# Optimization experiments

Hardware: AMD Instinct MI355X
Metric: run time of the kernel (lower is better)

The kernel has to match this reference:

```python
import jax, jax.numpy as jnp
import numpy as np

# config constants
H = 1024          # hidden_size
I = 512           # moe_intermediate_size
IS = 1024         # moe_shared_expert_intermediate_size
E = 16            # n_routed_experts
G = 4             # n_group
TOPK_G = 2        # topk_group
TOPK = 4          # num_experts_per_tok
SCALE = 2.5       # routed_scaling_factor
B, S = 2, 1024


def _relu2(x):
    r = jax.nn.relu(x)
    return r * r


def setup_inputs() -> dict:
    key = jax.random.key(0)
    ks = jax.random.split(key, 8)
    sd = 0.02
    return {
        "hidden_states": jax.random.normal(ks[0], (B, S, H), jnp.float32),
        "Wg": jax.random.normal(ks[1], (E, H), jnp.float32) * sd,          # router gate weight
        "bias_corr": jax.random.normal(ks[2], (E,), jnp.float32) * 0.01,    # e_score_correction_bias
        "W1": jax.random.normal(ks[3], (E, I, H), jnp.float32) * sd,        # experts up_proj
        "W2": jax.random.normal(ks[4], (E, H, I), jnp.float32) * sd,        # experts down_proj
        "Ws1": jax.random.normal(ks[5], (IS, H), jnp.float32) * sd,         # shared up_proj
        "Ws2": jax.random.normal(ks[6], (H, IS), jnp.float32) * sd,         # shared down_proj
    }


def _route(scores, bias_corr):
    # scores: (T,E) = sigmoid(router logits)
    T = scores.shape[0]
    s_choice = scores + bias_corr                                           # (T,E)
    gs = s_choice.reshape(T, G, E // G)
    group_scores = jnp.sum(jax.lax.top_k(gs, 2)[0], axis=-1)                # (T,G) sum of top-2 per group
    gidx = jax.lax.top_k(group_scores, TOPK_G)[1]                           # (T,topk_group)
    gmask = jnp.sum(jax.nn.one_hot(gidx, G, dtype=scores.dtype), axis=1)    # (T,G)
    smask = jnp.repeat(gmask, E // G, axis=1)                               # (T,E)
    masked = jnp.where(smask > 0, s_choice, 0.0)
    topk_idx = jax.lax.top_k(masked, TOPK)[1]                               # (T,top_k)
    topk_w = jnp.take_along_axis(scores, topk_idx, axis=1)                  # weights from raw sigmoid scores
    topk_w = topk_w / (jnp.sum(topk_w, axis=-1, keepdims=True) + 1e-20)     # norm_topk_prob
    topk_w = topk_w * SCALE
    return topk_idx, topk_w


def reference(hidden_states, Wg, bias_corr, W1, W2, Ws1, Ws2):
    b, s, h = hidden_states.shape
    flat = hidden_states.reshape(-1, h)                                     # (T,H)
    T = flat.shape[0]
    logits = flat.astype(jnp.float32) @ Wg.T                                # (T,E)
    scores = jax.nn.sigmoid(logits)
    topk_idx, topk_w = _route(scores, bias_corr)
    topk_w = topk_w.astype(hidden_states.dtype)
    # combined per-(token, expert) weight; zero where not routed (equivalent
    # to the per-expert gather/MLP/weighted index_add in the original)
    cw = jnp.zeros((T, E), flat.dtype)
    cw = cw.at[jnp.arange(T)[:, None], topk_idx].add(topk_w)                # (T,E)
    # fc1_latent_proj / fc2_latent_proj are Identity (moe_latent_size=None)
    hid = _relu2(jnp.einsum('th,eih->eti', flat, W1))                       # (E,T,I)
    y = jnp.einsum('eti,ehi->eth', hid, W2)                                 # (E,T,H)
    out = jnp.einsum('eth,te->th', y, cw)                                   # (T,H)
    shared = _relu2(flat @ Ws1.T) @ Ws2.T                                   # shared expert on residuals
    return (out + shared).reshape(b, s, h)
```

## Files before the change

### kernel.cpp

```cpp
#include <hip/hip_runtime.h>
#include <hip/hip_bf16.h>

#define T_TOK 2048
#define HDIM 1024
#define IDIM 512
#define ISDIM 1024
#define NEXP 16
#define TOPK 4
#define NSLOT (T_TOK*TOPK)
#define SCALE_F 2.5f

typedef unsigned short u16;
typedef float f32x4 __attribute__((ext_vector_type(4)));
typedef __bf16 bf16x8 __attribute__((ext_vector_type(8)));
typedef u16 u16x8 __attribute__((ext_vector_type(8)));

__device__ __forceinline__ u16 f2bf(float f) {
  unsigned u = __builtin_bit_cast(unsigned, f);
  u += 0x7fffu + ((u >> 16) & 1u);
  return (u16)(u >> 16);
}

__device__ __forceinline__ float bf2f(u16 h) {
  unsigned u = ((unsigned)h) << 16;
  return __builtin_bit_cast(float, u);
}

__device__ __forceinline__ void gload_lds16(const u16* g, u16* l) {
  __builtin_amdgcn_global_load_lds(
      (const __attribute__((address_space(1))) void*)g,
      (__attribute__((address_space(3))) void*)l, 16, 0, 0);
}

__device__ __forceinline__ f32x4 mfma16(u16x8 a, u16x8 b, f32x4 c) {
  return __builtin_amdgcn_mfma_f32_16x16x32_bf16(
      __builtin_bit_cast(bf16x8, a), __builtin_bit_cast(bf16x8, b), c, 0, 0, 0);
}

__device__ __forceinline__ void wait_vm6()   { asm volatile("s_waitcnt vmcnt(6)" ::: "memory"); }
__device__ __forceinline__ void wait_vm0()   { asm volatile("s_waitcnt vmcnt(0)" ::: "memory"); }
__device__ __forceinline__ void wait_lgkm0() { asm volatile("s_waitcnt lgkmcnt(0)" ::: "memory"); }

#define JMAX0 136
#define G0T (8*JMAX0)
#define JMAX1 240
#define G1T (8*JMAX1)
#define MAXG0 96
#define MAXG1 192

__global__ void __launch_bounds__(256) router_kernel(
    const float* __restrict__ x, const float* __restrict__ Wg,
    const float* __restrict__ bias,
    int* __restrict__ topk_idx, float* __restrict__ topk_w,
    u16* __restrict__ Xbf,
    int* __restrict__ counts, int* __restrict__ gfill) {
  int t = blockIdx.x;
  int tid = threadIdx.x;
  int lane = tid & 63;
  int wave = tid >> 6;

  if (t == 0 && tid < NEXP) { counts[tid] = 0; gfill[tid] = 0; }

  __shared__ __align__(16) float sx[HDIM];
  __shared__ float ssc[NEXP];

  float4 xv = reinterpret_cast<const float4*>(x + (size_t)t * HDIM)[tid];
  reinterpret_cast<float4*>(sx)[tid] = xv;
  ushort4 o;
  o.x = f2bf(xv.x); o.y = f2bf(xv.y); o.z = f2bf(xv.z); o.w = f2bf(xv.w);
  reinterpret_cast<ushort4*>(Xbf + (size_t)t * HDIM)[tid] = o;
  __syncthreads();

  float acc[4] = {0.f, 0.f, 0.f, 0.f};
  const float4* sx4 = reinterpret_cast<const float4*>(sx);
#pragma unroll
  for (int c = 0; c < 4; c++) {
    float4 xq = sx4[lane + 64 * c];
#pragma unroll
    for (int e = 0; e < 4; e++) {
      float4 wq = reinterpret_cast<const float4*>(
          Wg + (size_t)(wave * 4 + e) * HDIM)[lane + 64 * c];
      acc[e] += xq.x * wq.x + xq.y * wq.y + xq.z * wq.z + xq.w * wq.w;
    }
  }
#pragma unroll
  for (int e = 0; e < 4; e++) {
    float v = acc[e];
#pragma unroll
    for (int off = 32; off > 0; off >>= 1) v += __shfl_xor(v, off);
    if (lane == 0) ssc[wave * 4 + e] = v;
  }
  __syncthreads();

  if (tid == 0) {
    float scores[NEXP], sc[NEXP];
#pragma unroll
    for (int e = 0; e < NEXP; e++) {
      float s = 1.f / (1.f + expf(-ssc[e]));
      scores[e] = s;
      sc[e] = s + bias[e];
    }
    float gsum[4];
#pragma unroll
    for (int g = 0; g < 4; g++) {
      float a = sc[4*g], b = sc[4*g+1], c = sc[4*g+2], d = sc[4*g+3];
      float hi1 = fmaxf(a, b), lo1 = fminf(a, b);
      float hi2 = fmaxf(c, d), lo2 = fminf(c, d);
      gsum[g] = fmaxf(hi1, hi2) + fmaxf(fminf(hi1, hi2), fmaxf(lo1, lo2));
    }
    int g0 = 0; float bv = gsum[0];
#pragma unroll
    for (int g = 1; g < 4; g++) if (gsum[g] > bv) { bv = gsum[g]; g0 = g; }
    int g1 = -1; float bv2 = -1e30f;
#pragma unroll
    for (int g = 0; g < 4; g++) if (g != g0 && gsum[g] > bv2) { bv2 = gsum[g]; g1 = g; }
    float m[NEXP];
#pragma unroll
    for (int e = 0; e < NEXP; e++) {
      int g = e >> 2;
      m[e] = (g == g0 || g == g1) ? sc[e] : 0.0f;
    }
    int idx[TOPK]; float w[TOPK];
#pragma unroll
    for (int k = 0; k < TOPK; k++) {
      int bj = 0; float bmv = m[0];
#pragma unroll
      for (int j = 1; j < NEXP; j++) if (m[j] > bmv) { bmv = m[j]; bj = j; }
      idx[k] = bj; w[k] = scores[bj];
#pragma unroll
      for (int j = 0; j < NEXP; j++) m[j] = (j == bj) ? -1e30f : m[j];
    }
    float s4 = w[0] + w[1] + w[2] + w[3] + 1e-20f;
    float inv = SCALE_F / s4;
#pragma unroll
    for (int k = 0; k < TOPK; k++) {
      topk_idx[t * TOPK + k] = idx[k];
      topk_w[t * TOPK + k] = w[k] * inv;
    }
  }
}

__global__ void __launch_bounds__(256) hist_kernel(
    const int* __restrict__ topk_idx, int* __restrict__ counts) {
  int j = blockIdx.x * 256 + threadIdx.x;
  int lane = threadIdx.x & 63;
  int e = topk_idx[j];
  unsigned long long m = ~0ull;
#pragma unroll
  for (int b = 0; b < 4; b++) {
    unsigned long long bb = __ballot((e >> b) & 1);
    m &= ((e >> b) & 1) ? bb : ~bb;
  }
  int leader = __ffsll(m) - 1;
  if (lane == leader) atomicAdd(&counts[e], __popcll(m));
}

__global__ void __launch_bounds__(256) scatter_build(
    const int* __restrict__ topk_idx, const float* __restrict__ topk_w,
    const int* __restrict__ counts, int* __restrict__ offsets,
    int* __restrict__ gfill,
    int* __restrict__ perm_token, float* __restrict__ perm_w,
    int* __restrict__ slot_of,
    int* __restrict__ tiles0, int* __restrict__ tiles1) {
  int b = blockIdx.x;
  int tid = threadIdx.x;
  int lane = tid & 63;

  if (b < 32) {
    int c = (lane < NEXP) ? counts[lane] : 0;
    int incl = c;
#pragma unroll
    for (int o = 1; o < 16; o <<= 1) {
      int v = __shfl_up(incl, o);
      if (lane >= o) incl += v;
    }
    int excl = incl - c;

    int j = b * 256 + tid;
    int e = topk_idx[j];
    unsigned long long m = ~0ull;
#pragma unroll
    for (int bb = 0; bb < 4; bb++) {
      unsigned long long bl = __ballot((e >> bb) & 1);
      m &= ((e >> bb) & 1) ? bl : ~bl;
    }
    int leader = __ffsll(m) - 1;
    int rank = __popcll(m & ((1ull << lane) - 1ull));
    int base = 0;
    if (lane == leader) base = atomicAdd(&gfill[e], __popcll(m));
    base = __shfl(base, leader);
    int pos = __shfl(excl, e) + base + rank;
    perm_token[pos] = j >> 2;
    perm_w[pos] = topk_w[j];
    slot_of[j] = pos;
    if (b == 0 && tid < NEXP) offsets[tid] = excl;
    return;
  }

  __shared__ int hcnt[NEXP];
  __shared__ int g0s[MAXG0], g0c[MAXG0], g0n[MAXG0];
  __shared__ int g1s[MAXG1], g1c[MAXG1], g1n[MAXG1];
  __shared__ int sng0, sng1;
  if (tid < NEXP) hcnt[tid] = counts[tid];
  __syncthreads();

  if (tid == 0) {
    int l0=0,l1=0,l2=0,l3=0,l4=0,l5=0,l6=0,l7=0;
    int ng = 0;
#define PLACE0(code0, cn)                                               \
    { int x = 0, lv = l0;                                               \
      if (l1<lv){lv=l1;x=1;} if (l2<lv){lv=l2;x=2;}                     \
      if (l3<lv){lv=l3;x=3;} if (l4<lv){lv=l4;x=4;}                     \
      if (l5<lv){lv=l5;x=5;} if (l6<lv){lv=l6;x=6;}                     \
      if (l7<lv){lv=l7;x=7;}                                            \
      g0s[ng] = x + 8*lv; g0c[ng] = (code0); g0n[ng] = (cn); ng++;      \
      if (x==0)l0+=(cn); else if (x==1)l1+=(cn); else if (x==2)l2+=(cn);\
      else if (x==3)l3+=(cn); else if (x==4)l4+=(cn);                   \
      else if (x==5)l5+=(cn); else if (x==6)l6+=(cn); else l7+=(cn); }
    for (int nb = 0; nb < 8; nb++) PLACE0((16 << 10) | nb, 32);
    for (int e = 0; e < NEXP; e++) {
      int mc = (hcnt[e] + 63) >> 6;
      for (int nb = 0; nb < 4; nb++)
        for (int base = 0; base < mc; base += 32)
          PLACE0((e << 10) | (base << 3) | nb, min(32, mc - base));
    }
    sng0 = ng;
#undef PLACE0
  }
  if (tid == 64) {
    int l0=0,l1=0,l2=0,l3=0,l4=0,l5=0,l6=0,l7=0;
    int ng = 0;
#define PLACE1(code0, cn)                                               \
    { int x = 0, lv = l0;                                               \
      if (l1<lv){lv=l1;x=1;} if (l2<lv){lv=l2;x=2;}                     \
      if (l3<lv){lv=l3;x=3;} if (l4<lv){lv=l4;x=4;}                     \
      if (l5<lv){lv=l5;x=5;} if (l6<lv){lv=l6;x=6;}                     \
      if (l7<lv){lv=l7;x=7;}                                            \
      g1s[ng] = x + 8*lv; g1c[ng] = (code0); g1n[ng] = (cn); ng++;      \
      if (x==0)l0+=(cn); else if (x==1)l1+=(cn); else if (x==2)l2+=(cn);\
      else if (x==3)l3+=(cn); else if (x==4)l4+=(cn);                   \
      else if (x==5)l5+=(cn); else if (x==6)l6+=(cn); else l7+=(cn); }
    for (int eh = 16; eh <= 17; eh++)
      for (int nb = 0; nb < 8; nb++) PLACE1((eh << 10) | nb, 32);
    for (int e = 0; e < NEXP; e++) {
      int mc = (hcnt[e] + 63) >> 6;
      for (int nb = 0; nb < 8; nb++)
        for (int base = 0; base < mc; base += 32)
          PLACE1((e << 10) | (base << 3) | nb, min(32, mc - base));
    }
    sng1 = ng;
#undef PLACE1
  }
  if (tid >= 128) {
    for (int i = tid - 128; i < G0T; i += 128) tiles0[i] = -1;
    for (int i = tid - 128; i < G1T; i += 128) tiles1[i] = -1;
  }
  __syncthreads();

  int ng0 = sng0, ng1 = sng1;
  for (int g = tid; g < ng0; g += 256) {
    int st = g0s[g], c0 = g0c[g], cn = g0n[g];
    for (int mm = 0; mm < cn; mm++) tiles0[st + 8 * mm] = c0 + (mm << 3);
  }
  for (int g = tid; g < ng1; g += 256) {
    int st = g1s[g], c0 = g1c[g], cn = g1n[g];
    for (int mm = 0; mm < cn; mm++) tiles1[st + 8 * mm] = c0 + (mm << 3);
  }
}

#define N1Q (NEXP*IDIM*HDIM/4)
#define NSQ (ISDIM*HDIM/4)
__global__ void __launch_bounds__(256) cvt_all(
    const float* __restrict__ W1, const float* __restrict__ W2,
    const float* __restrict__ Ws1, const float* __restrict__ Ws2,
    u16* __restrict__ W1b, u16* __restrict__ W2b,
    u16* __restrict__ Ws1b, u16* __restrict__ Ws2b) {
  int i = blockIdx.x * 256 + threadIdx.x;
  const float* src; u16* dst; int off;
  if (i < N1Q)               { src = W1;  dst = W1b;  off = i; }
  else if (i < 2 * N1Q)      { src = W2;  dst = W2b;  off = i - N1Q; }
  else if (i < 2 * N1Q + NSQ){ src = Ws1; dst = Ws1b; off = i - 2 * N1Q; }
  else                       { src = Ws2; dst = Ws2b; off = i - 2 * N1Q - NSQ; }
  float4 v = reinterpret_cast<const float4*>(src)[off];
  ushort4 o;
  o.x = f2bf(v.x); o.y = f2bf(v.y); o.z = f2bf(v.z); o.w = f2bf(v.w);
  reinterpret_cast<ushort4*>(dst)[off] = o;
}

#define BM 64
#define BN 128
#define BK 64

template<int PHASE>
__global__ void __launch_bounds__(256) moe_gemm(
    const int* __restrict__ tiles,
    const u16* __restrict__ Xbf, const u16* __restrict__ Hg,
    const u16* __restrict__ Hs,
    const u16* __restrict__ W1b, const u16* __restrict__ W2b,
    const u16* __restrict__ Ws1b, const u16* __restrict__ Ws2b,
    const int* __restrict__ eoffs, const int* __restrict__ ecnts,
    const int* __restrict__ rowmap, const float* __restrict__ rowscale,
    u16* __restrict__ HgOut, u16* __restrict__ HsOut,
    u16* __restrict__ Ygb, float* __restrict__ Ys)
{
  constexpr int KL = (PHASE == 0) ? HDIM : IDIM;
  constexpr int NT = KL / BK;

  int code = tiles[blockIdx.x];
  if (code < 0) return;
  int e  = code >> 10;
  int mb = (code >> 3) & 127;
  int nb = code & 7;

  bool sh = (e >= NEXP);
  int half = e - NEXP;
  int N, Mloc, rowbase, Astr, Bstr, kb;
  const u16* Abase;
  const u16* Bp;
  if (PHASE == 0) {
    Astr = HDIM; Bstr = HDIM; kb = 0;
    if (sh) { N = ISDIM; Mloc = T_TOK; rowbase = 0; Abase = Xbf; Bp = Ws1b; }
    else    { N = IDIM; Mloc = ecnts[e]; rowbase = eoffs[e]; Abase = Xbf;
              Bp = W1b + (size_t)e * IDIM * HDIM; }
  } else {
    N = HDIM;
    if (sh) { Astr = ISDIM; Bstr = ISDIM; kb = half * IDIM;
              Mloc = T_TOK; rowbase = 0; Abase = Hs; Bp = Ws2b; }
    else    { Astr = IDIM; Bstr = IDIM; kb = 0;
              Mloc = ecnts[e]; rowbase = eoffs[e]; Abase = Hg;
              Bp = W2b + (size_t)e * HDIM * IDIM; }
  }
  int m0 = mb * BM;
  if (m0 >= Mloc) return;
  int n0 = nb * BN;
  if (n0 >= N) return;

  __shared__ __align__(16) u16 sA[2][BM * BK];
  __shared__ __align__(16) u16 sB[2][BN * BK];

  int tid = threadIdx.x;
  int lane = tid & 63;
  int wave = tid >> 6;
  int wm = (wave >> 1) * 32;
  int wn = (wave & 1) * 64;
  int fm = lane & 15;
  int kq = lane >> 4;
  int fsw = fm & 7;

  int lrow8 = lane >> 3;
  int sch = ((lane & 7) ^ lrow8) * 8;

  const u16* AgP[2];
  int aoff[2];
#pragma unroll
  for (int g = 0; g < 2; g++) {
    int rt = 16 * wave + 8 * g + lrow8;
    int ar = m0 + rt;
    int arc = (ar < Mloc) ? ar : (Mloc - 1);
    size_t asrc;
    if (PHASE == 0 && !sh) asrc = (size_t)rowmap[rowbase + arc] * Astr;
    else                   asrc = (size_t)((sh ? 0 : rowbase) + arc) * Astr;
    AgP[g] = Abase + asrc + kb + sch;
    aoff[g] = (16 * wave + 8 * g) * BK;
  }
  const u16* BgP[4];
  int boff[4];
#pragma unroll
  for (int g = 0; g < 4; g++) {
    int rt = 32 * wave + 8 * g + lrow8;
    BgP[g] = Bp + (size_t)(n0 + rt) * Bstr + kb + sch;
    boff[g] = (32 * wave + 8 * g) * BK;
  }

  f32x4 acc[2][4] = {};

#pragma unroll
  for (int g = 0; g < 2; g++) gload_lds16(AgP[g], &sA[0][aoff[g]]);
#pragma unroll
  for (int g = 0; g < 4; g++) gload_lds16(BgP[g], &sB[0][boff[g]]);
#pragma unroll
  for (int g = 0; g < 2; g++) gload_lds16(AgP[g] + BK, &sA[1][aoff[g]]);
#pragma unroll
  for (int g = 0; g < 4; g++) gload_lds16(BgP[g] + BK, &sB[1][boff[g]]);

  for (int t = 0; t < NT - 1; ++t) {
    int cur = t & 1;
    wait_vm6();
    __builtin_amdgcn_s_barrier();
    u16x8 af[2][2], bf[2][4];
#pragma unroll
    for (int ks = 0; ks < 2; ks++) {
      int ch = ((ks * 4 + kq) ^ fsw) * 8;
#pragma unroll
      for (int i = 0; i < 2; i++)
        af[ks][i] = *reinterpret_cast<const u16x8*>(&sA[cur][(wm + 16 * i + fm) * BK + ch]);
#pragma unroll
      for (int j = 0; j < 4; j++)
        bf[ks][j] = *reinterpret_cast<const u16x8*>(&sB[cur][(wn + 16 * j + fm) * BK + ch]);
    }
    wait_lgkm0();
    __builtin_amdgcn_sched_barrier(0);
    __builtin_amdgcn_s_barrier();
    if (t + 2 < NT) {
#pragma unroll
      for (int g = 0; g < 2; g++) gload_lds16(AgP[g] + (t + 2) * BK, &sA[cur][aoff[g]]);
#pragma unroll
      for (int g = 0; g < 4; g++) gload_lds16(BgP[g] + (t + 2) * BK, &sB[cur][boff[g]]);
    }
#pragma unroll
    for (int ks = 0; ks < 2; ks++)
#pragma unroll
      for (int i = 0; i < 2; i++)
#pragma unroll
        for (int j = 0; j < 4; j++)
          acc[i][j] = mfma16(af[ks][i], bf[ks][j], acc[i][j]);
  }
  {
    constexpr int cur = (NT - 1) & 1;
    wait_vm0();
    __builtin_amdgcn_s_barrier();
    u16x8 af[2][2], bf[2][4];
#pragma unroll
    for (int ks = 0; ks < 2; ks++) {
      int ch = ((ks * 4 + kq) ^ fsw) * 8;
#pragma unroll
      for (int i = 0; i < 2; i++)
        af[ks][i] = *reinterpret_cast<const u16x8*>(&sA[cur][(wm + 16 * i + fm) * BK + ch]);
#pragma unroll
      for (int j = 0; j < 4; j++)
        bf[ks][j] = *reinterpret_cast<const u16x8*>(&sB[cur][(wn + 16 * j + fm) * BK + ch]);
    }
    wait_lgkm0();
    __builtin_amdgcn_sched_barrier(0);
#pragma unroll
    for (int ks = 0; ks < 2; ks++)
#pragma unroll
      for (int i = 0; i < 2; i++)
#pragma unroll
        for (int j = 0; j < 4; j++)
          acc[i][j] = mfma16(af[ks][i], bf[ks][j], acc[i][j]);
  }

#pragma unroll
  for (int i = 0; i < 2; i++) {
#pragma unroll
    for (int r = 0; r < 4; r++) {
      int gm = m0 + wm + 16 * i + kq * 4 + r;
      if (gm < Mloc) {
        float rs = 0.f;
        if (PHASE == 0 && !sh) rs = rowscale[rowbase + gm];
#pragma unroll
        for (int j = 0; j < 4; j++) {
          int gn = n0 + wn + 16 * j + fm;
          float v = acc[i][j][r];
          if (PHASE == 0) {
            float tq = fmaxf(v, 0.f);
            if (!sh) {
              tq = tq * tq * rs;
              HgOut[(size_t)(rowbase + gm) * IDIM + gn] = f2bf(tq);
            } else {
              HsOut[(size_t)gm * ISDIM + gn] = f2bf(tq * tq);
            }
          } else {
            if (!sh) Ygb[(size_t)(rowbase + gm) * HDIM + gn] = f2bf(v);
            else     Ys[(size_t)(half * T_TOK + gm) * HDIM + gn] = v;
          }
        }
      }
    }
  }
}

__global__ void __launch_bounds__(256) combine_kernel(
    const u16* __restrict__ Ygb, const float* __restrict__ Ys,
    const int* __restrict__ slot_of, float* __restrict__ out) {
  int t = blockIdx.x;
  int i = threadIdx.x;
  int4 s = *reinterpret_cast<const int4*>(&slot_of[t * 4]);
  const ushort4* Y4 = reinterpret_cast<const ushort4*>(Ygb);
  const float4* S4 = reinterpret_cast<const float4*>(Ys);
  float4* O4 = reinterpret_cast<float4*>(out);
  float4 v0 = S4[(size_t)t * 256 + i];
  float4 v1 = S4[(size_t)(T_TOK + t) * 256 + i];
  ushort4 a = Y4[(size_t)s.x * 256 + i];
  ushort4 b = Y4[(size_t)s.y * 256 + i];
  ushort4 c = Y4[(size_t)s.z * 256 + i];
  ushort4 d = Y4[(size_t)s.w * 256 + i];
  float4 v;
  v.x = v0.x + v1.x + bf2f(a.x) + bf2f(b.x) + bf2f(c.x) + bf2f(d.x);
  v.y = v0.y + v1.y + bf2f(a.y) + bf2f(b.y) + bf2f(c.y) + bf2f(d.y);
  v.z = v0.z + v1.z + bf2f(a.z) + bf2f(b.z) + bf2f(c.z) + bf2f(d.z);
  v.w = v0.w + v1.w + bf2f(a.w) + bf2f(b.w) + bf2f(c.w) + bf2f(d.w);
  O4[(size_t)t * 256 + i] = v;
}

extern "C" void kernel_launch(void* const* d_in, const int* in_sizes, int n_in,
                              void* d_out, int out_size, void* d_ws, size_t ws_size,
                              hipStream_t stream) {
  const float* x    = (const float*)d_in[0];
  const float* Wg   = (const float*)d_in[1];
  const float* bias = (const float*)d_in[2];
  const float* W1   = (const float*)d_in[3];
  const float* W2   = (const float*)d_in[4];
  const float* Ws1  = (const float*)d_in[5];
  const float* Ws2  = (const float*)d_in[6];
  float* out = (float*)d_out;

  char* p = (char*)d_ws;
  auto alloc = [&](size_t bytes) -> void* {
    void* r = (void*)p;
    p += (bytes + 255) & ~(size_t)255;
    return r;
  };
  int*   topk_idx   = (int*)  alloc((size_t)NSLOT * 4);
  float* topk_w     = (float*)alloc((size_t)NSLOT * 4);
  int*   counts     = (int*)  alloc(64);
  int*   offsets    = (int*)  alloc(64);
  int*   gfill      = (int*)  alloc(64);
  int*   perm_token = (int*)  alloc((size_t)NSLOT * 4);
  float* perm_w     = (float*)alloc((size_t)NSLOT * 4);
  int*   slot_of    = (int*)  alloc((size_t)NSLOT * 4);
  int*   tiles0     = (int*)  alloc((size_t)G0T * 4);
  int*   tiles1     = (int*)  alloc((size_t)G1T * 4);
  u16*   Xbf        = (u16*)  alloc((size_t)T_TOK * HDIM * 2);
  u16*   W1b        = (u16*)  alloc((size_t)NEXP * IDIM * HDIM * 2);
  u16*   W2b        = (u16*)  alloc((size_t)NEXP * HDIM * IDIM * 2);
  u16*   Ws1b      = (u16*)  alloc((size_t)ISDIM * HDIM * 2);
  u16*   Ws2b      = (u16*)  alloc((size_t)HDIM * ISDIM * 2);
  u16*   Hg         = (u16*)  alloc((size_t)NSLOT * IDIM * 2);
  u16*   Hs         = (u16*)  alloc((size_t)T_TOK * ISDIM * 2);
  u16*   Ygb        = (u16*)  alloc((size_t)NSLOT * HDIM * 2);
  float* Ys         = (float*)alloc((size_t)2 * T_TOK * HDIM * 4);

  router_kernel<<<T_TOK, 256, 0, stream>>>(x, Wg, bias, topk_idx, topk_w, Xbf,
                                           counts, gfill);
  hist_kernel<<<32, 256, 0, stream>>>(topk_idx, counts);
  scatter_build<<<33, 256, 0, stream>>>(topk_idx, topk_w, counts, offsets,
                                        gfill, perm_token, perm_w, slot_of,
                                        tiles0, tiles1);

  cvt_all<<<(2 * N1Q + 2 * NSQ + 255) / 256, 256, 0, stream>>>(
      W1, W2, Ws1, Ws2, W1b, W2b, Ws1b, Ws2b);

  moe_gemm<0><<<G0T, 256, 0, stream>>>(
      tiles0, Xbf, Hg, Hs, W1b, W2b, Ws1b, Ws2b, offsets, counts,
      perm_token, perm_w, Hg, Hs, nullptr, nullptr);

  moe_gemm<1><<<G1T, 256, 0, stream>>>(
      tiles1, Xbf, Hg, Hs, W1b, W2b, Ws1b, Ws2b, offsets, counts,
      perm_token, perm_w, Hg, Hs, Ygb, Ys);

  combine_kernel<<<T_TOK, 256, 0, stream>>>(Ygb, Ys, slot_of, out);
}
```

Measured before the change: 234.6 us.

## Fuse fp32-to-bf16 weight conversion into MoE GEMM loads via register staging

Removes the standalone weight conversion kernel and its bf16 weight buffers; the GEMM kernels now load fp32 weight tiles into registers, convert to bf16, and write them into swizzled LDS. The A operand keeps async global-to-LDS loads but the pipeline becomes single-step prefetch with a full vmem wait per iteration. This saves a full pass over all weights per call but doubles weight bytes per tile load and reduces latency hiding in the GEMM main loop.

```diff
diff --git a/kernel.cpp b/kernel.cpp
--- a/kernel.cpp
+++ b/kernel.cpp
@@ -37,7 +37,6 @@
       __builtin_bit_cast(bf16x8, a), __builtin_bit_cast(bf16x8, b), c, 0, 0, 0);
 }
 
-__device__ __forceinline__ void wait_vm6()   { asm volatile("s_waitcnt vmcnt(6)" ::: "memory"); }
 __device__ __forceinline__ void wait_vm0()   { asm volatile("s_waitcnt vmcnt(0)" ::: "memory"); }
 __device__ __forceinline__ void wait_lgkm0() { asm volatile("s_waitcnt lgkmcnt(0)" ::: "memory"); }
 
@@ -268,25 +267,6 @@
   }
 }
 
-#define N1Q (NEXP*IDIM*HDIM/4)
-#define NSQ (ISDIM*HDIM/4)
-__global__ void __launch_bounds__(256) cvt_all(
-    const float* __restrict__ W1, const float* __restrict__ W2,
-    const float* __restrict__ Ws1, const float* __restrict__ Ws2,
-    u16* __restrict__ W1b, u16* __restrict__ W2b,
-    u16* __restrict__ Ws1b, u16* __restrict__ Ws2b) {
-  int i = blockIdx.x * 256 + threadIdx.x;
-  const float* src; u16* dst; int off;
-  if (i < N1Q)               { src = W1;  dst = W1b;  off = i; }
-  else if (i < 2 * N1Q)      { src = W2;  dst = W2b;  off = i - N1Q; }
-  else if (i < 2 * N1Q + NSQ){ src = Ws1; dst = Ws1b; off = i - 2 * N1Q; }
-  else                       { src = Ws2; dst = Ws2b; off = i - 2 * N1Q - NSQ; }
-  float4 v = reinterpret_cast<const float4*>(src)[off];
-  ushort4 o;
-  o.x = f2bf(v.x); o.y = f2bf(v.y); o.z = f2bf(v.z); o.w = f2bf(v.w);
-  reinterpret_cast<ushort4*>(dst)[off] = o;
-}
-
 #define BM 64
 #define BN 128
 #define BK 64
@@ -296,8 +276,8 @@
     const int* __restrict__ tiles,
     const u16* __restrict__ Xbf, const u16* __restrict__ Hg,
     const u16* __restrict__ Hs,
-    const u16* __restrict__ W1b, const u16* __restrict__ W2b,
-    const u16* __restrict__ Ws1b, const u16* __restrict__ Ws2b,
+    const float* __restrict__ W1, const float* __restrict__ W2,
+    const float* __restrict__ Ws1, const float* __restrict__ Ws2,
     const int* __restrict__ eoffs, const int* __restrict__ ecnts,
     const int* __restrict__ rowmap, const float* __restrict__ rowscale,
     u16* __restrict__ HgOut, u16* __restrict__ HsOut,
@@ -316,19 +296,19 @@
   int half = e - NEXP;
   int N, Mloc, rowbase, Astr, Bstr, kb;
   const u16* Abase;
-  const u16* Bp;
+  const float* Bp;
   if (PHASE == 0) {
     Astr = HDIM; Bstr = HDIM; kb = 0;
-    if (sh) { N = ISDIM; Mloc = T_TOK; rowbase = 0; Abase = Xbf; Bp = Ws1b; }
+    if (sh) { N = ISDIM; Mloc = T_TOK; rowbase = 0; Abase = Xbf; Bp = Ws1; }
     else    { N = IDIM; Mloc = ecnts[e]; rowbase = eoffs[e]; Abase = Xbf;
-              Bp = W1b + (size_t)e * IDIM * HDIM; }
+              Bp = W1 + (size_t)e * IDIM * HDIM; }
   } else {
     N = HDIM;
     if (sh) { Astr = ISDIM; Bstr = ISDIM; kb = half * IDIM;
-              Mloc = T_TOK; rowbase = 0; Abase = Hs; Bp = Ws2b; }
+              Mloc = T_TOK; rowbase = 0; Abase = Hs; Bp = Ws2; }
     else    { Astr = IDIM; Bstr = IDIM; kb = 0;
               Mloc = ecnts[e]; rowbase = eoffs[e]; Abase = Hg;
-              Bp = W2b + (size_t)e * HDIM * IDIM; }
+              Bp = W2 + (size_t)e * HDIM * IDIM; }
   }
   int m0 = mb * BM;
   if (m0 >= Mloc) return;
@@ -348,7 +328,8 @@
   int fsw = fm & 7;
 
   int lrow8 = lane >> 3;
-  int sch = ((lane & 7) ^ lrow8) * 8;
+  int lch = lane & 7;
+  int sch = (lch ^ lrow8) * 8;
 
   const u16* AgP[2];
   int aoff[2];
@@ -363,30 +344,49 @@
     AgP[g] = Abase + asrc + kb + sch;
     aoff[g] = (16 * wave + 8 * g) * BK;
   }
-  const u16* BgP[4];
-  int boff[4];
+  const float* BgPf[4];
+  int boffw[4];
 #pragma unroll
   for (int g = 0; g < 4; g++) {
     int rt = 32 * wave + 8 * g + lrow8;
-    BgP[g] = Bp + (size_t)(n0 + rt) * Bstr + kb + sch;
-    boff[g] = (32 * wave + 8 * g) * BK;
+    BgPf[g] = Bp + (size_t)(n0 + rt) * Bstr + kb + lch * 8;
+    boffw[g] = (32 * wave + 8 * g + lrow8) * BK + sch;
   }
 
   f32x4 acc[2][4] = {};
+  f32x4 breg[4][2];
 
 #pragma unroll
   for (int g = 0; g < 2; g++) gload_lds16(AgP[g], &sA[0][aoff[g]]);
 #pragma unroll
-  for (int g = 0; g < 4; g++) gload_lds16(BgP[g], &sB[0][boff[g]]);
-#pragma unroll
-  for (int g = 0; g < 2; g++) gload_lds16(AgP[g] + BK, &sA[1][aoff[g]]);
-#pragma unroll
-  for (int g = 0; g < 4; g++) gload_lds16(BgP[g] + BK, &sB[1][boff[g]]);
-
-  for (int t = 0; t < NT - 1; ++t) {
+  for (int g = 0; g < 4; g++) {
+    breg[g][0] = *reinterpret_cast<const f32x4*>(BgPf[g]);
+    breg[g][1] = *reinterpret_cast<const f32x4*>(BgPf[g] + 4);
+  }
+  wait_vm0();
+#pragma unroll
+  for (int g = 0; g < 4; g++) {
+    u16x8 o;
+#pragma unroll
+    for (int q = 0; q < 4; q++) { o[q] = f2bf(breg[g][0][q]); o[4+q] = f2bf(breg[g][1][q]); }
+    *reinterpret_cast<u16x8*>(&sB[0][boffw[g]]) = o;
+  }
+  wait_lgkm0();
+  __builtin_amdgcn_s_barrier();
+
+  for (int t = 0; t < NT; ++t) {
     int cur = t & 1;
-    wait_vm6();
-    __builtin_amdgcn_s_barrier();
+    int nxt = cur ^ 1;
+    if (t + 1 < NT) {
+#pragma unroll
+      for (int g = 0; g < 2; g++)
+        gload_lds16(AgP[g] + (t + 1) * BK, &sA[nxt][aoff[g]]);
+#pragma unroll
+      for (int g = 0; g < 4; g++) {
+        breg[g][0] = *reinterpret_cast<const f32x4*>(BgPf[g] + (t + 1) * BK);
+        breg[g][1] = *reinterpret_cast<const f32x4*>(BgPf[g] + (t + 1) * BK + 4);
+      }
+    }
     u16x8 af[2][2], bf[2][4];
 #pragma unroll
     for (int ks = 0; ks < 2; ks++) {
@@ -400,13 +400,6 @@
     }
     wait_lgkm0();
     __builtin_amdgcn_sched_barrier(0);
-    __builtin_amdgcn_s_barrier();
-    if (t + 2 < NT) {
-#pragma unroll
-      for (int g = 0; g < 2; g++) gload_lds16(AgP[g] + (t + 2) * BK, &sA[cur][aoff[g]]);
-#pragma unroll
-      for (int g = 0; g < 4; g++) gload_lds16(BgP[g] + (t + 2) * BK, &sB[cur][boff[g]]);
-    }
 #pragma unroll
     for (int ks = 0; ks < 2; ks++)
 #pragma unroll
@@ -414,31 +407,18 @@
 #pragma unroll
         for (int j = 0; j < 4; j++)
           acc[i][j] = mfma16(af[ks][i], bf[ks][j], acc[i][j]);
-  }
-  {
-    constexpr int cur = (NT - 1) & 1;
-    wait_vm0();
+    if (t + 1 < NT) {
+      wait_vm0();
+#pragma unroll
+      for (int g = 0; g < 4; g++) {
+        u16x8 o;
+#pragma unroll
+        for (int q = 0; q < 4; q++) { o[q] = f2bf(breg[g][0][q]); o[4+q] = f2bf(breg[g][1][q]); }
+        *reinterpret_cast<u16x8*>(&sB[nxt][boffw[g]]) = o;
+      }
+      wait_lgkm0();
+    }
     __builtin_amdgcn_s_barrier();
-    u16x8 af[2][2], bf[2][4];
-#pragma unroll
-    for (int ks = 0; ks < 2; ks++) {
-      int ch = ((ks * 4 + kq) ^ fsw) * 8;
-#pragma unroll
-      for (int i = 0; i < 2; i++)
-        af[ks][i] = *reinterpret_cast<const u16x8*>(&sA[cur][(wm + 16 * i + fm) * BK + ch]);
-#pragma unroll
-      for (int j = 0; j < 4; j++)
-        bf[ks][j] = *reinterpret_cast<const u16x8*>(&sB[cur][(wn + 16 * j + fm) * BK + ch]);
-    }
-    wait_lgkm0();
-    __builtin_amdgcn_sched_barrier(0);
-#pragma unroll
-    for (int ks = 0; ks < 2; ks++)
-#pragma unroll
-      for (int i = 0; i < 2; i++)
-#pragma unroll
-        for (int j = 0; j < 4; j++)
-          acc[i][j] = mfma16(af[ks][i], bf[ks][j], acc[i][j]);
   }
 
 #pragma unroll
@@ -523,10 +503,6 @@
   int*   tiles0     = (int*)  alloc((size_t)G0T * 4);
   int*   tiles1     = (int*)  alloc((size_t)G1T * 4);
   u16*   Xbf        = (u16*)  alloc((size_t)T_TOK * HDIM * 2);
-  u16*   W1b        = (u16*)  alloc((size_t)NEXP * IDIM * HDIM * 2);
-  u16*   W2b        = (u16*)  alloc((size_t)NEXP * HDIM * IDIM * 2);
-  u16*   Ws1b      = (u16*)  alloc((size_t)ISDIM * HDIM * 2);
-  u16*   Ws2b      = (u16*)  alloc((size_t)HDIM * ISDIM * 2);
   u16*   Hg         = (u16*)  alloc((size_t)NSLOT * IDIM * 2);
   u16*   Hs         = (u16*)  alloc((size_t)T_TOK * ISDIM * 2);
   u16*   Ygb        = (u16*)  alloc((size_t)NSLOT * HDIM * 2);
@@ -539,15 +515,12 @@
                                         gfill, perm_token, perm_w, slot_of,
                                         tiles0, tiles1);
 
-  cvt_all<<<(2 * N1Q + 2 * NSQ + 255) / 256, 256, 0, stream>>>(
-      W1, W2, Ws1, Ws2, W1b, W2b, Ws1b, Ws2b);
-
   moe_gemm<0><<<G0T, 256, 0, stream>>>(
-      tiles0, Xbf, Hg, Hs, W1b, W2b, Ws1b, Ws2b, offsets, counts,
+      tiles0, Xbf, Hg, Hs, W1, W2, Ws1, Ws2, offsets, counts,
       perm_token, perm_w, Hg, Hs, nullptr, nullptr);
 
   moe_gemm<1><<<G1T, 256, 0, stream>>>(
-      tiles1, Xbf, Hg, Hs, W1b, W2b, Ws1b, Ws2b, offsets, counts,
+      tiles1, Xbf, Hg, Hs, W1, W2, Ws1, Ws2, offsets, counts,
       perm_token, perm_w, Hg, Hs, Ygb, Ys);
 
   combine_kernel<<<T_TOK, 256, 0, stream>>>(Ygb, Ys, slot_of, out);
```

After: 267.3 us. +13.9%, slower.

## Fold weight conversions into router and phase-0 GEMM launches to overlap work

Applied to the files above, without the earlier changes.

Removes the standalone weight-conversion kernel. W1/Ws1 fp32→bf16 conversion now runs as extra blocks of the router kernel, and W2/Ws2 conversion runs as extra blocks of the phase-0 GEMM. The aim is to overlap the memory-bound conversion with the router and GEMM work and to cut one launch. The cost is that the extra blocks compete for CUs with the GEMM tiles, and block scheduling order may delay GEMM progress.

```diff
diff --git a/kernel.cpp b/kernel.cpp
--- a/kernel.cpp
+++ b/kernel.cpp
@@ -48,14 +48,36 @@
 #define MAXG0 96
 #define MAXG1 192
 
+#define N1Q (NEXP*IDIM*HDIM/4)
+#define N2Q (NEXP*HDIM*IDIM/4)
+#define NSQ (ISDIM*HDIM/4)
+#define CVTB ((N1Q + NSQ) / 256)
+
+__device__ __forceinline__ void cvt_f4(const float* src, u16* dst, int off) {
+  float4 v = reinterpret_cast<const float4*>(src)[off];
+  ushort4 o;
+  o.x = f2bf(v.x); o.y = f2bf(v.y); o.z = f2bf(v.z); o.w = f2bf(v.w);
+  reinterpret_cast<ushort4*>(dst)[off] = o;
+}
+
 __global__ void __launch_bounds__(256) router_kernel(
     const float* __restrict__ x, const float* __restrict__ Wg,
     const float* __restrict__ bias,
     int* __restrict__ topk_idx, float* __restrict__ topk_w,
     u16* __restrict__ Xbf,
-    int* __restrict__ counts, int* __restrict__ gfill) {
+    int* __restrict__ counts, int* __restrict__ gfill,
+    const float* __restrict__ W1, const float* __restrict__ Ws1,
+    u16* __restrict__ W1b, u16* __restrict__ Ws1b) {
   int t = blockIdx.x;
   int tid = threadIdx.x;
+
+  if (t >= T_TOK) {
+    int i = (t - T_TOK) * 256 + tid;
+    if (i < N1Q) cvt_f4(W1, W1b, i);
+    else         cvt_f4(Ws1, Ws1b, i - N1Q);
+    return;
+  }
+
   int lane = tid & 63;
   int wave = tid >> 6;
 
@@ -268,25 +290,6 @@
   }
 }
 
-#define N1Q (NEXP*IDIM*HDIM/4)
-#define NSQ (ISDIM*HDIM/4)
-__global__ void __launch_bounds__(256) cvt_all(
-    const float* __restrict__ W1, const float* __restrict__ W2,
-    const float* __restrict__ Ws1, const float* __restrict__ Ws2,
-    u16* __restrict__ W1b, u16* __restrict__ W2b,
-    u16* __restrict__ Ws1b, u16* __restrict__ Ws2b) {
-  int i = blockIdx.x * 256 + threadIdx.x;
-  const float* src; u16* dst; int off;
-  if (i < N1Q)               { src = W1;  dst = W1b;  off = i; }
-  else if (i < 2 * N1Q)      { src = W2;  dst = W2b;  off = i - N1Q; }
-  else if (i < 2 * N1Q + NSQ){ src = Ws1; dst = Ws1b; off = i - 2 * N1Q; }
-  else                       { src = Ws2; dst = Ws2b; off = i - 2 * N1Q - NSQ; }
-  float4 v = reinterpret_cast<const float4*>(src)[off];
-  ushort4 o;
-  o.x = f2bf(v.x); o.y = f2bf(v.y); o.z = f2bf(v.z); o.w = f2bf(v.w);
-  reinterpret_cast<ushort4*>(dst)[off] = o;
-}
-
 #define BM 64
 #define BN 128
 #define BK 64
@@ -298,6 +301,8 @@
     const u16* __restrict__ Hs,
     const u16* __restrict__ W1b, const u16* __restrict__ W2b,
     const u16* __restrict__ Ws1b, const u16* __restrict__ Ws2b,
+    const float* __restrict__ W2f, const float* __restrict__ Ws2f,
+    u16* __restrict__ W2bo, u16* __restrict__ Ws2bo,
     const int* __restrict__ eoffs, const int* __restrict__ ecnts,
     const int* __restrict__ rowmap, const float* __restrict__ rowscale,
     u16* __restrict__ HgOut, u16* __restrict__ HsOut,
@@ -305,6 +310,13 @@
 {
   constexpr int KL = (PHASE == 0) ? HDIM : IDIM;
   constexpr int NT = KL / BK;
+
+  if (PHASE == 0 && blockIdx.x >= G0T) {
+    int i = (blockIdx.x - G0T) * 256 + threadIdx.x;
+    if (i < N2Q) cvt_f4(W2f, W2bo, i);
+    else         cvt_f4(Ws2f, Ws2bo, i - N2Q);
+    return;
+  }
 
   int code = tiles[blockIdx.x];
   if (code < 0) return;
@@ -532,23 +544,21 @@
   u16*   Ygb        = (u16*)  alloc((size_t)NSLOT * HDIM * 2);
   float* Ys         = (float*)alloc((size_t)2 * T_TOK * HDIM * 4);
 
-  router_kernel<<<T_TOK, 256, 0, stream>>>(x, Wg, bias, topk_idx, topk_w, Xbf,
-                                           counts, gfill);
+  router_kernel<<<T_TOK + CVTB, 256, 0, stream>>>(
+      x, Wg, bias, topk_idx, topk_w, Xbf, counts, gfill,
+      W1, Ws1, W1b, Ws1b);
   hist_kernel<<<32, 256, 0, stream>>>(topk_idx, counts);
   scatter_build<<<33, 256, 0, stream>>>(topk_idx, topk_w, counts, offsets,
                                         gfill, perm_token, perm_w, slot_of,
                                         tiles0, tiles1);
 
-  cvt_all<<<(2 * N1Q + 2 * NSQ + 255) / 256, 256, 0, stream>>>(
-      W1, W2, Ws1, Ws2, W1b, W2b, Ws1b, Ws2b);
-
-  moe_gemm<0><<<G0T, 256, 0, stream>>>(
-      tiles0, Xbf, Hg, Hs, W1b, W2b, Ws1b, Ws2b, offsets, counts,
-      perm_token, perm_w, Hg, Hs, nullptr, nullptr);
+  moe_gemm<0><<<G0T + CVTB, 256, 0, stream>>>(
+      tiles0, Xbf, Hg, Hs, W1b, W2b, Ws1b, Ws2b, W2, Ws2, W2b, Ws2b,
+      offsets, counts, perm_token, perm_w, Hg, Hs, nullptr, nullptr);
 
   moe_gemm<1><<<G1T, 256, 0, stream>>>(
-      tiles1, Xbf, Hg, Hs, W1b, W2b, Ws1b, Ws2b, offsets, counts,
-      perm_token, perm_w, Hg, Hs, Ygb, Ys);
+      tiles1, Xbf, Hg, Hs, W1b, W2b, Ws1b, Ws2b, W2, Ws2, W2b, Ws2b,
+      offsets, counts, perm_token, perm_w, Hg, Hs, Ygb, Ys);
 
   combine_kernel<<<T_TOK, 256, 0, stream>>>(Ygb, Ys, slot_of, out);
 }
```

Result: faster. 227.5 us (-3.0%).
